# Optimization experiments

Hardware: AMD Instinct MI355X
Metric: run time of the kernel (lower is better)

The kernel has to match this reference:

```python
import jax, jax.numpy as jnp
import numpy as np

N = 16384
D = 512
VOCAB = 100000
EMB_SCALE = 0.05  # keep dot products ~O(1) so exp() is stable, like trained embeddings


def setup_inputs() -> dict:
    key = jax.random.key(0)
    k1, k2, k3, k4 = jax.random.split(key, 4)
    input_emb = jax.random.normal(k1, (N, D), dtype=jnp.float32) * EMB_SCALE
    target_emb = jax.random.normal(k2, (N, D), dtype=jnp.float32) * EMB_SCALE
    target_ids = jax.random.randint(k3, (N,), 0, VOCAB, dtype=jnp.int64) if jax.config.jax_enable_x64 else jax.random.randint(k3, (N,), 0, VOCAB, dtype=jnp.int32)
    # sampling probabilities in (eps, ~0.5) so 1 - q stays well away from 0
    q_probas = jax.random.uniform(k4, (N,), dtype=jnp.float32, minval=1e-4, maxval=0.5)
    # first half positives, second half negatives (static pattern, matches boolean-mask semantics)
    mask = jnp.arange(N) < (N // 2)
    return {"input_emb": input_emb, "target_emb": target_emb, "target_ids": target_ids,
            "q_probas": q_probas, "mask": mask}


def reference(input_emb, target_emb, target_ids, q_probas, mask):
    # mask is a constant selection pattern -> resolve to static index lists (jit-friendly shapes)
    mask_np = np.asarray(mask)
    pos_idx = np.nonzero(mask_np)[0]
    neg_idx = np.nonzero(~mask_np)[0]

    pos_emb = input_emb[pos_idx]                      # [P, D]
    pos_tgt = target_emb[pos_idx]                     # [P, D]
    neg_tgt = target_emb[neg_idx]                     # [Q, D]

    pos_sim = jnp.einsum('pd,pd->p', pos_emb, pos_tgt)          # [P]
    neg_sim = jnp.einsum('pd,qd->pq', pos_emb, neg_tgt)         # [P, Q]

    # accidental-hit mask: 1 where negative id differs from the positive's true id
    miss = (target_ids[pos_idx][:, None] != target_ids[neg_idx]).astype(jnp.float32)  # [P, Q]
    n_miss = jnp.sum(miss, axis=1, keepdims=True)                # [P, 1]

    # logQ correction: subtract log(n_miss * q_neg / (1 - q_pos))
    log_q = jnp.log(n_miss * q_probas[neg_idx][None, :] / (1.0 - q_probas[pos_idx][:, None]))
    neg_exp = jnp.exp(neg_sim - log_q)                           # [P, Q]
    neg_exp_sum = jnp.einsum('pq,pq->p', miss, neg_exp)          # [P]

    pos_exp = jnp.exp(pos_sim)
    batch_loss = jnp.mean(-pos_sim + jnp.log(pos_exp + neg_exp_sum))
    return batch_loss
```

## Files before the change

kernel.cpp:

```cpp
#include <hip/hip_runtime.h>
#include <hip/hip_bf16.h>

#define NPOS 8192
#define NNEG 8192
#define DIM  512
#define VOCAB 100000

#define FP8_SCALE 64.0f
#define ACC_DESCALE (1.0f / 4096.0f)

typedef float f32x4 __attribute__((ext_vector_type(4)));
typedef long  lng2  __attribute__((ext_vector_type(2)));

__device__ __forceinline__ void async_load16(const void* g, void* l) {
    __builtin_amdgcn_global_load_lds(
        (const __attribute__((address_space(1))) void*)g,
        (__attribute__((address_space(3))) void*)l, 16, 0, 0);
}

__global__ void prep_kernel(const float* __restrict__ input_emb,
                            const float* __restrict__ target_emb,
                            const int* __restrict__ ids,
                            const float* __restrict__ q_probas,
                            unsigned char* __restrict__ A8,
                            unsigned char* __restrict__ B8,
                            float* __restrict__ w, float* __restrict__ pos_sim,
                            int* __restrict__ hist) {
    const int r    = (blockIdx.x * blockDim.x + threadIdx.x) >> 6;
    const int lane = threadIdx.x & 63;

    const float4* ain = (const float4*)(input_emb  + (size_t)r * DIM);
    const float4* tin = (const float4*)(target_emb + (size_t)r * DIM);
    const float4* bin = (const float4*)(target_emb + (size_t)(NPOS + r) * DIM);

    float4 a0 = ain[lane * 2], a1 = ain[lane * 2 + 1];
    float4 t0 = tin[lane * 2], t1 = tin[lane * 2 + 1];
    float4 b0 = bin[lane * 2], b1 = bin[lane * 2 + 1];

    int alo = __builtin_amdgcn_cvt_pk_fp8_f32(a0.x * FP8_SCALE, a0.y * FP8_SCALE, 0, false);
    alo     = __builtin_amdgcn_cvt_pk_fp8_f32(a0.z * FP8_SCALE, a0.w * FP8_SCALE, alo, true);
    int ahi = __builtin_amdgcn_cvt_pk_fp8_f32(a1.x * FP8_SCALE, a1.y * FP8_SCALE, 0, false);
    ahi     = __builtin_amdgcn_cvt_pk_fp8_f32(a1.z * FP8_SCALE, a1.w * FP8_SCALE, ahi, true);
    int blo = __builtin_amdgcn_cvt_pk_fp8_f32(b0.x * FP8_SCALE, b0.y * FP8_SCALE, 0, false);
    blo     = __builtin_amdgcn_cvt_pk_fp8_f32(b0.z * FP8_SCALE, b0.w * FP8_SCALE, blo, true);
    int bhi = __builtin_amdgcn_cvt_pk_fp8_f32(b1.x * FP8_SCALE, b1.y * FP8_SCALE, 0, false);
    bhi     = __builtin_amdgcn_cvt_pk_fp8_f32(b1.z * FP8_SCALE, b1.w * FP8_SCALE, bhi, true);

    const int s = lane & 7, wnd = lane >> 3;
    const int phys = wnd * 64 + (s & 3) * 16 + (s >> 2) * 8;
    *(int2*)(A8 + (size_t)r * DIM + phys) = make_int2(alo, ahi);
    *(int2*)(B8 + (size_t)r * DIM + phys) = make_int2(blo, bhi);

    float sum = a0.x * t0.x + a0.y * t0.y + a0.z * t0.z + a0.w * t0.w
              + a1.x * t1.x + a1.y * t1.y + a1.z * t1.z + a1.w * t1.w;
    #pragma unroll
    for (int m = 32; m >= 1; m >>= 1) sum += __shfl_xor(sum, m);

    if (lane == 0) {
        pos_sim[r] = sum;
        w[r] = 1.0f / q_probas[NPOS + r];
        atomicAdd(&hist[ids[NPOS + r]], 1);
    }
}

__global__ __launch_bounds__(256) void gemm_kernel(
        const unsigned char* __restrict__ A8, const unsigned char* __restrict__ B8,
        const int* __restrict__ ids, const float* __restrict__ w,
        float* __restrict__ S) {
    __shared__ __align__(16) unsigned char Atile[2][128 * 64];
    __shared__ __align__(16) unsigned char Btile[2][128 * 64];

    const int tid  = threadIdx.x;
    const int lane = tid & 63;
    const int wv   = tid >> 6;
    const int wave_m = (wv & 1) * 64;
    const int wave_n = (wv >> 1) * 64;
    const int quad = lane >> 4;
    const int r16  = lane & 15;
    const int bm = blockIdx.x, bn = blockIdx.y;

    f32x4 acc[4][4] = {};

    const int srow_in = lane >> 2;
    const int sgran   = (lane & 3) ^ ((lane >> 3) & 3);
    const int row0 = wv * 32 + srow_in;
    const int row1 = wv * 32 + 16 + srow_in;
    const size_t goff0 = (size_t)row0 * DIM + sgran * 16;
    const size_t goff1 = (size_t)row1 * DIM + sgran * 16;
    const unsigned char* a_src = A8 + (size_t)(bm * 128) * DIM;
    const unsigned char* b_src = B8 + (size_t)(bn * 128) * DIM;
    const int ldst0 = (wv * 2) * 1024;
    const int ldst1 = (wv * 2 + 1) * 1024;

    async_load16(a_src + goff0, Atile[0] + ldst0);
    async_load16(a_src + goff1, Atile[0] + ldst1);
    async_load16(b_src + goff0, Btile[0] + ldst0);
    async_load16(b_src + goff1, Btile[0] + ldst1);
    __syncthreads();

    const int slot = quad ^ ((r16 >> 1) & 3);
    for (int it = 0; it < 8; ++it) {
        const int cur = it & 1;
        if (it < 7) {
            const size_t kb = (size_t)(it + 1) * 64;
            async_load16(a_src + kb + goff0, Atile[cur ^ 1] + ldst0);
            async_load16(a_src + kb + goff1, Atile[cur ^ 1] + ldst1);
            async_load16(b_src + kb + goff0, Btile[cur ^ 1] + ldst0);
            async_load16(b_src + kb + goff1, Btile[cur ^ 1] + ldst1);
        }

        lng2 af[4], bg[4];
        #pragma unroll
        for (int i = 0; i < 4; ++i) {
            const int arow = wave_m + i * 16 + r16;
            af[i] = *(const lng2*)(Atile[cur] + arow * 64 + slot * 16);
            const int brow = wave_n + i * 16 + r16;
            bg[i] = *(const lng2*)(Btile[cur] + brow * 64 + slot * 16);
        }
        #pragma unroll
        for (int i = 0; i < 4; ++i)
            #pragma unroll
            for (int j = 0; j < 4; ++j)
                acc[i][j] = __builtin_amdgcn_mfma_f32_16x16x32_fp8_fp8(af[i].x, bg[j].x, acc[i][j], 0, 0, 0);
        #pragma unroll
        for (int i = 0; i < 4; ++i)
            #pragma unroll
            for (int j = 0; j < 4; ++j)
                acc[i][j] = __builtin_amdgcn_mfma_f32_16x16x32_fp8_fp8(af[i].y, bg[j].y, acc[i][j], 0, 0, 0);

        if (it < 7) __syncthreads();
    }

    int idq[4]; float wq[4];
    #pragma unroll
    for (int j = 0; j < 4; ++j) {
        const int q = bn * 128 + wave_n + j * 16 + r16;
        idq[j] = ids[NPOS + q];
        wq[j]  = w[q];
    }
    #pragma unroll
    for (int i = 0; i < 4; ++i) {
        const int p0 = bm * 128 + wave_m + i * 16 + quad * 4;
        #pragma unroll
        for (int rr = 0; rr < 4; ++rr) {
            const int p = p0 + rr;
            const int idp = ids[p];
            float partial = 0.f;
            #pragma unroll
            for (int j = 0; j < 4; ++j) {
                const float e = __expf(acc[i][j][rr] * ACC_DESCALE) * wq[j];
                partial += (idp != idq[j]) ? e : 0.f;
            }
            partial += __shfl_xor(partial, 1);
            partial += __shfl_xor(partial, 2);
            partial += __shfl_xor(partial, 4);
            partial += __shfl_xor(partial, 8);
            if (r16 == 0) atomicAdd(&S[p], partial);
        }
    }
}

__global__ void final_kernel(const float* __restrict__ pos_sim,
                             const float* __restrict__ S,
                             const int* __restrict__ hist,
                             const int* __restrict__ ids,
                             const float* __restrict__ q_probas,
                             float* __restrict__ out) {
    __shared__ float red[256];
    float local = 0.f;
    for (int p = threadIdx.x; p < NPOS; p += 256) {
        const float ps  = pos_sim[p];
        const float n_miss = (float)(NNEG - hist[ids[p]]);
        const float nes = S[p] * (1.0f - q_probas[p]) / n_miss;
        local += -ps + logf(expf(ps) + nes);
    }
    red[threadIdx.x] = local;
    __syncthreads();
    #pragma unroll
    for (int s = 128; s > 0; s >>= 1) {
        if (threadIdx.x < s) red[threadIdx.x] += red[threadIdx.x + s];
        __syncthreads();
    }
    if (threadIdx.x == 0) out[0] = red[0] / (float)NPOS;
}

extern "C" void kernel_launch(void* const* d_in, const int* in_sizes, int n_in,
                              void* d_out, int out_size, void* d_ws, size_t ws_size,
                              hipStream_t stream) {
    const float* input_emb  = (const float*)d_in[0];
    const float* target_emb = (const float*)d_in[1];
    const int*   target_ids = (const int*)d_in[2];
    const float* q_probas   = (const float*)d_in[3];

    char* ws = (char*)d_ws;
    unsigned char* A8 = (unsigned char*)ws;
    unsigned char* B8 = (unsigned char*)(ws + (size_t)NPOS * DIM);
    float*  S       = (float*)(ws + (size_t)NPOS * DIM * 2);
    int*    hist    = (int*)(S + NPOS);
    float*  w       = (float*)(hist + VOCAB);
    float*  pos_sim = w + NPOS;

    hipMemsetAsync(S, 0, (size_t)(NPOS + VOCAB) * 4, stream);
    prep_kernel<<<2048, 256, 0, stream>>>(input_emb, target_emb, target_ids,
                                          q_probas, A8, B8, w, pos_sim, hist);
    gemm_kernel<<<dim3(64, 64), 256, 0, stream>>>(A8, B8, target_ids, w, S);
    final_kernel<<<1, 256, 0, stream>>>(pos_sim, S, hist, target_ids, q_probas, (float*)d_out);
}
```

Before: 208.7 us.

## Switch GEMM to scaled 32x32x64 FP8 MFMA with triple-buffered LDS pipeline

Replaces the 16x16x32 FP8 MFMA tiles with the MI355X block-scaled 32x32x64 f8f6f4 MFMA, using E8M0 scale operands to fold the descale into the instruction. The A/B FP8 layout written by the prep kernel becomes linear, and LDS reads use a new swizzle. The K loop moves from double to triple buffering with explicit vmcnt waits and a single barrier per step, plus setprio around the MFMAs. This aims to raise matrix throughput and cut synchronisation stalls, at the cost of more LDS use and correctness depending on the MFMA lane layout and the scale encoding.

```diff
diff --git a/kernel.cpp b/kernel.cpp
--- a/kernel.cpp
+++ b/kernel.cpp
@@ -7,10 +7,11 @@
 #define VOCAB 100000
 
 #define FP8_SCALE 64.0f
-#define ACC_DESCALE (1.0f / 4096.0f)
-
-typedef float f32x4 __attribute__((ext_vector_type(4)));
-typedef long  lng2  __attribute__((ext_vector_type(2)));
+#define SCALE_E8M0 0x79797979
+
+typedef int   i32x4  __attribute__((ext_vector_type(4)));
+typedef int   i32x8  __attribute__((ext_vector_type(8)));
+typedef float f32x16 __attribute__((ext_vector_type(16)));
 
 __device__ __forceinline__ void async_load16(const void* g, void* l) {
     __builtin_amdgcn_global_load_lds(
@@ -46,10 +47,8 @@
     int bhi = __builtin_amdgcn_cvt_pk_fp8_f32(b1.x * FP8_SCALE, b1.y * FP8_SCALE, 0, false);
     bhi     = __builtin_amdgcn_cvt_pk_fp8_f32(b1.z * FP8_SCALE, b1.w * FP8_SCALE, bhi, true);
 
-    const int s = lane & 7, wnd = lane >> 3;
-    const int phys = wnd * 64 + (s & 3) * 16 + (s >> 2) * 8;
-    *(int2*)(A8 + (size_t)r * DIM + phys) = make_int2(alo, ahi);
-    *(int2*)(B8 + (size_t)r * DIM + phys) = make_int2(blo, bhi);
+    *(int2*)(A8 + (size_t)r * DIM + lane * 8) = make_int2(alo, ahi);
+    *(int2*)(B8 + (size_t)r * DIM + lane * 8) = make_int2(blo, bhi);
 
     float sum = a0.x * t0.x + a0.y * t0.y + a0.z * t0.z + a0.w * t0.w
               + a1.x * t1.x + a1.y * t1.y + a1.z * t1.z + a1.w * t1.w;
@@ -67,19 +66,19 @@
         const unsigned char* __restrict__ A8, const unsigned char* __restrict__ B8,
         const int* __restrict__ ids, const float* __restrict__ w,
         float* __restrict__ S) {
-    __shared__ __align__(16) unsigned char Atile[2][128 * 64];
-    __shared__ __align__(16) unsigned char Btile[2][128 * 64];
+    __shared__ __align__(16) unsigned char Atile[3][128 * 64];
+    __shared__ __align__(16) unsigned char Btile[3][128 * 64];
 
     const int tid  = threadIdx.x;
     const int lane = tid & 63;
     const int wv   = tid >> 6;
     const int wave_m = (wv & 1) * 64;
     const int wave_n = (wv >> 1) * 64;
-    const int quad = lane >> 4;
-    const int r16  = lane & 15;
+    const int h    = lane >> 5;
+    const int r32  = lane & 31;
     const int bm = blockIdx.x, bn = blockIdx.y;
 
-    f32x4 acc[4][4] = {};
+    f32x16 acc[2][2] = {};
 
     const int srow_in = lane >> 2;
     const int sgran   = (lane & 3) ^ ((lane >> 3) & 3);
@@ -96,66 +95,86 @@
     async_load16(a_src + goff1, Atile[0] + ldst1);
     async_load16(b_src + goff0, Btile[0] + ldst0);
     async_load16(b_src + goff1, Btile[0] + ldst1);
-    __syncthreads();
-
-    const int slot = quad ^ ((r16 >> 1) & 3);
+    async_load16(a_src + 64 + goff0, Atile[1] + ldst0);
+    async_load16(a_src + 64 + goff1, Atile[1] + ldst1);
+    async_load16(b_src + 64 + goff0, Btile[1] + ldst0);
+    async_load16(b_src + 64 + goff1, Btile[1] + ldst1);
+
+    #pragma unroll
     for (int it = 0; it < 8; ++it) {
-        const int cur = it & 1;
-        if (it < 7) {
-            const size_t kb = (size_t)(it + 1) * 64;
-            async_load16(a_src + kb + goff0, Atile[cur ^ 1] + ldst0);
-            async_load16(a_src + kb + goff1, Atile[cur ^ 1] + ldst1);
-            async_load16(b_src + kb + goff0, Btile[cur ^ 1] + ldst0);
-            async_load16(b_src + kb + goff1, Btile[cur ^ 1] + ldst1);
+        if (it < 7) asm volatile("s_waitcnt vmcnt(4)" ::: "memory");
+        else        asm volatile("s_waitcnt vmcnt(0)" ::: "memory");
+        __builtin_amdgcn_s_barrier();
+
+        if (it < 6) {
+            const size_t kb = (size_t)(it + 2) * 64;
+            unsigned char* At = Atile[(it + 2) % 3];
+            unsigned char* Bt = Btile[(it + 2) % 3];
+            async_load16(a_src + kb + goff0, At + ldst0);
+            async_load16(a_src + kb + goff1, At + ldst1);
+            async_load16(b_src + kb + goff0, Bt + ldst0);
+            async_load16(b_src + kb + goff1, Bt + ldst1);
         }
 
-        lng2 af[4], bg[4];
+        const unsigned char* At = Atile[it % 3];
+        const unsigned char* Bt = Btile[it % 3];
+        i32x8 af[2], bg[2];
         #pragma unroll
-        for (int i = 0; i < 4; ++i) {
-            const int arow = wave_m + i * 16 + r16;
-            af[i] = *(const lng2*)(Atile[cur] + arow * 64 + slot * 16);
-            const int brow = wave_n + i * 16 + r16;
-            bg[i] = *(const lng2*)(Btile[cur] + brow * 64 + slot * 16);
+        for (int i = 0; i < 2; ++i) {
+            const int arow = wave_m + i * 32 + r32;
+            const int s0 = (((h << 1) ^ ((arow >> 1) & 3)) * 16);
+            const unsigned char* ap = At + arow * 64;
+            i32x4 alo = *(const i32x4*)(ap + s0);
+            i32x4 ahi = *(const i32x4*)(ap + (s0 ^ 16));
+            af[i].lo = alo; af[i].hi = ahi;
+            const int brow = wave_n + i * 32 + r32;
+            const int t0 = (((h << 1) ^ ((brow >> 1) & 3)) * 16);
+            const unsigned char* bp = Bt + brow * 64;
+            i32x4 blo = *(const i32x4*)(bp + t0);
+            i32x4 bhi = *(const i32x4*)(bp + (t0 ^ 16));
+            bg[i].lo = blo; bg[i].hi = bhi;
         }
+
+        __builtin_amdgcn_s_setprio(1);
         #pragma unroll
-        for (int i = 0; i < 4; ++i)
+        for (int i = 0; i < 2; ++i)
             #pragma unroll
-            for (int j = 0; j < 4; ++j)
-                acc[i][j] = __builtin_amdgcn_mfma_f32_16x16x32_fp8_fp8(af[i].x, bg[j].x, acc[i][j], 0, 0, 0);
-        #pragma unroll
-        for (int i = 0; i < 4; ++i)
-            #pragma unroll
-            for (int j = 0; j < 4; ++j)
-                acc[i][j] = __builtin_amdgcn_mfma_f32_16x16x32_fp8_fp8(af[i].y, bg[j].y, acc[i][j], 0, 0, 0);
-
-        if (it < 7) __syncthreads();
-    }
-
-    int idq[4]; float wq[4];
-    #pragma unroll
-    for (int j = 0; j < 4; ++j) {
-        const int q = bn * 128 + wave_n + j * 16 + r16;
+            for (int j = 0; j < 2; ++j)
+                acc[i][j] = __builtin_amdgcn_mfma_scale_f32_32x32x64_f8f6f4(
+                    af[i], bg[j], acc[i][j], 0, 0,
+                    0, SCALE_E8M0, 0, SCALE_E8M0);
+        __builtin_amdgcn_s_setprio(0);
+
+        asm volatile("s_waitcnt lgkmcnt(0)" ::: "memory");
+        __builtin_amdgcn_sched_barrier(0);
+    }
+
+    int idq[2]; float wq[2];
+    #pragma unroll
+    for (int j = 0; j < 2; ++j) {
+        const int q = bn * 128 + wave_n + j * 32 + r32;
         idq[j] = ids[NPOS + q];
         wq[j]  = w[q];
     }
     #pragma unroll
-    for (int i = 0; i < 4; ++i) {
-        const int p0 = bm * 128 + wave_m + i * 16 + quad * 4;
+    for (int i = 0; i < 2; ++i) {
+        const int p_base = bm * 128 + wave_m + i * 32 + 4 * h;
         #pragma unroll
-        for (int rr = 0; rr < 4; ++rr) {
-            const int p = p0 + rr;
+        for (int reg = 0; reg < 16; ++reg) {
+            const int p = p_base + (reg & 3) + 8 * (reg >> 2);
             const int idp = ids[p];
             float partial = 0.f;
             #pragma unroll
-            for (int j = 0; j < 4; ++j) {
-                const float e = __expf(acc[i][j][rr] * ACC_DESCALE) * wq[j];
+            for (int j = 0; j < 2; ++j) {
+                const float e = __expf(acc[i][j][reg]) * wq[j];
                 partial += (idp != idq[j]) ? e : 0.f;
             }
             partial += __shfl_xor(partial, 1);
             partial += __shfl_xor(partial, 2);
             partial += __shfl_xor(partial, 4);
             partial += __shfl_xor(partial, 8);
-            if (r16 == 0) atomicAdd(&S[p], partial);
+            partial += __shfl_xor(partial, 16);
+            if (r32 == 0) atomicAdd(&S[p], partial);
         }
     }
 }
```

After: 436.5 us. +109.1%, slower.

## Enlarge GEMM tile to 256x256 with 8 waves and ping-pong staged MFMA pipeline

Applied to the files above, without the earlier changes.

Doubles the block tile to 256x256 with 512 threads (8 waves, each owning 128x64), which halves global re-reads per output. The K loop is split into four MFMA phases separated by barriers, and async LDS loads for later k-tiles are interleaved between them, with s_setprio raising priority during MFMA bursts. The goal is to overlap loads with matrix math in a ping-pong style. It raises register pressure (acc[8][4]), doubles LDS use, and cuts the grid to 1024 blocks, which risks lower occupancy and more barrier overhead.

```diff
diff --git a/kernel.cpp b/kernel.cpp
--- a/kernel.cpp
+++ b/kernel.cpp
@@ -63,93 +63,128 @@
     }
 }
 
-__global__ __launch_bounds__(256) void gemm_kernel(
+__global__ __launch_bounds__(512, 2) void gemm_kernel(
         const unsigned char* __restrict__ A8, const unsigned char* __restrict__ B8,
         const int* __restrict__ ids, const float* __restrict__ w,
         float* __restrict__ S) {
-    __shared__ __align__(16) unsigned char Atile[2][128 * 64];
-    __shared__ __align__(16) unsigned char Btile[2][128 * 64];
+    __shared__ __align__(16) unsigned char Atile[2][256 * 64];
+    __shared__ __align__(16) unsigned char Btile[2][256 * 64];
 
     const int tid  = threadIdx.x;
     const int lane = tid & 63;
     const int wv   = tid >> 6;
-    const int wave_m = (wv & 1) * 64;
-    const int wave_n = (wv >> 1) * 64;
+    const int wm   = wv >> 2;
+    const int wn   = wv & 3;
     const int quad = lane >> 4;
     const int r16  = lane & 15;
     const int bm = blockIdx.x, bn = blockIdx.y;
 
-    f32x4 acc[4][4] = {};
-
-    const int srow_in = lane >> 2;
-    const int sgran   = (lane & 3) ^ ((lane >> 3) & 3);
-    const int row0 = wv * 32 + srow_in;
-    const int row1 = wv * 32 + 16 + srow_in;
-    const size_t goff0 = (size_t)row0 * DIM + sgran * 16;
-    const size_t goff1 = (size_t)row1 * DIM + sgran * 16;
-    const unsigned char* a_src = A8 + (size_t)(bm * 128) * DIM;
-    const unsigned char* b_src = B8 + (size_t)(bn * 128) * DIM;
-    const int ldst0 = (wv * 2) * 1024;
-    const int ldst1 = (wv * 2 + 1) * 1024;
-
-    async_load16(a_src + goff0, Atile[0] + ldst0);
-    async_load16(a_src + goff1, Atile[0] + ldst1);
-    async_load16(b_src + goff0, Btile[0] + ldst0);
-    async_load16(b_src + goff1, Btile[0] + ldst1);
-    __syncthreads();
+    f32x4 acc[8][4] = {};
+
+    const int srow  = (wv << 4) + (lane >> 2);
+    const int sgran = (lane & 3) ^ ((lane >> 3) & 3);
+    const unsigned char* a_base = A8 + (size_t)(bm * 256) * DIM;
+    const unsigned char* b_base = B8 + (size_t)(bn * 256) * DIM;
+
+#define STAGE_A(kt, h) async_load16(a_base + (size_t)((h)*128 + srow)*DIM + (kt)*64 + sgran*16, \
+                                    Atile[(kt)&1] + (h)*8192 + (wv<<10))
+#define STAGE_B(kt, h) async_load16(b_base + (size_t)((h)*128 + srow)*DIM + (kt)*64 + sgran*16, \
+                                    Btile[(kt)&1] + (h)*8192 + (wv<<10))
+
+    STAGE_A(0, 0); STAGE_A(0, 1); STAGE_B(0, 0); STAGE_B(0, 1);
+    STAGE_A(1, 0); STAGE_B(1, 0); STAGE_B(1, 1);
+    asm volatile("s_waitcnt vmcnt(3)" ::: "memory");
+    __builtin_amdgcn_s_barrier();
 
     const int slot = quad ^ ((r16 >> 1) & 3);
-    for (int it = 0; it < 8; ++it) {
-        const int cur = it & 1;
-        if (it < 7) {
-            const size_t kb = (size_t)(it + 1) * 64;
-            async_load16(a_src + kb + goff0, Atile[cur ^ 1] + ldst0);
-            async_load16(a_src + kb + goff1, Atile[cur ^ 1] + ldst1);
-            async_load16(b_src + kb + goff0, Btile[cur ^ 1] + ldst0);
-            async_load16(b_src + kb + goff1, Btile[cur ^ 1] + ldst1);
-        }
-
-        lng2 af[4], bg[4];
-        #pragma unroll
-        for (int i = 0; i < 4; ++i) {
-            const int arow = wave_m + i * 16 + r16;
-            af[i] = *(const lng2*)(Atile[cur] + arow * 64 + slot * 16);
-            const int brow = wave_n + i * 16 + r16;
-            bg[i] = *(const lng2*)(Btile[cur] + brow * 64 + slot * 16);
-        }
-        #pragma unroll
-        for (int i = 0; i < 4; ++i)
-            #pragma unroll
-            for (int j = 0; j < 4; ++j)
-                acc[i][j] = __builtin_amdgcn_mfma_f32_16x16x32_fp8_fp8(af[i].x, bg[j].x, acc[i][j], 0, 0, 0);
-        #pragma unroll
-        for (int i = 0; i < 4; ++i)
-            #pragma unroll
-            for (int j = 0; j < 4; ++j)
-                acc[i][j] = __builtin_amdgcn_mfma_f32_16x16x32_fp8_fp8(af[i].y, bg[j].y, acc[i][j], 0, 0, 0);
-
-        if (it < 7) __syncthreads();
-    }
+    lng2 af03[4], af47[4], bg[4];
+
+    #pragma unroll
+    for (int kt = 0; kt < 8; ++kt) {
+        const unsigned char* At = Atile[kt & 1];
+        const unsigned char* Bt = Btile[kt & 1];
+
+        #pragma unroll
+        for (int f = 0; f < 4; ++f)
+            af03[f] = *(const lng2*)(At + (wm*128 + f*16 + r16)*64 + slot*16);
+        #pragma unroll
+        for (int n = 0; n < 4; ++n)
+            bg[n] = *(const lng2*)(Bt + (wn*64 + n*16 + r16)*64 + slot*16);
+        if (kt < 7) STAGE_A(kt + 1, 1);
+        __builtin_amdgcn_s_barrier();
+        asm volatile("s_waitcnt lgkmcnt(0)" ::: "memory");
+        __builtin_amdgcn_sched_barrier(0);
+        __builtin_amdgcn_s_setprio(1);
+        #pragma unroll
+        for (int f = 0; f < 4; ++f)
+            #pragma unroll
+            for (int n = 0; n < 4; ++n)
+                acc[f][n] = __builtin_amdgcn_mfma_f32_16x16x32_fp8_fp8(af03[f].x, bg[n].x, acc[f][n], 0, 0, 0);
+        __builtin_amdgcn_s_setprio(0);
+        __builtin_amdgcn_s_barrier();
+
+        #pragma unroll
+        for (int f = 0; f < 4; ++f)
+            af47[f] = *(const lng2*)(At + (wm*128 + (f+4)*16 + r16)*64 + slot*16);
+        if (kt < 6) STAGE_B(kt + 2, 0);
+        __builtin_amdgcn_s_barrier();
+        asm volatile("s_waitcnt lgkmcnt(0)" ::: "memory");
+        __builtin_amdgcn_sched_barrier(0);
+        __builtin_amdgcn_s_setprio(1);
+        #pragma unroll
+        for (int f = 0; f < 4; ++f)
+            #pragma unroll
+            for (int n = 0; n < 4; ++n)
+                acc[f+4][n] = __builtin_amdgcn_mfma_f32_16x16x32_fp8_fp8(af47[f].x, bg[n].x, acc[f+4][n], 0, 0, 0);
+        __builtin_amdgcn_s_setprio(0);
+        __builtin_amdgcn_s_barrier();
+
+        if (kt < 6) STAGE_B(kt + 2, 1);
+        __builtin_amdgcn_s_barrier();
+        __builtin_amdgcn_s_setprio(1);
+        #pragma unroll
+        for (int f = 0; f < 4; ++f)
+            #pragma unroll
+            for (int n = 0; n < 4; ++n)
+                acc[f][n] = __builtin_amdgcn_mfma_f32_16x16x32_fp8_fp8(af03[f].y, bg[n].y, acc[f][n], 0, 0, 0);
+        __builtin_amdgcn_s_setprio(0);
+        __builtin_amdgcn_s_barrier();
+
+        if (kt < 6) STAGE_A(kt + 2, 0);
+        __builtin_amdgcn_s_barrier();
+        __builtin_amdgcn_s_setprio(1);
+        #pragma unroll
+        for (int f = 0; f < 4; ++f)
+            #pragma unroll
+            for (int n = 0; n < 4; ++n)
+                acc[f+4][n] = __builtin_amdgcn_mfma_f32_16x16x32_fp8_fp8(af47[f].y, bg[n].y, acc[f+4][n], 0, 0, 0);
+        __builtin_amdgcn_s_setprio(0);
+        if (kt < 6)       asm volatile("s_waitcnt vmcnt(3)" ::: "memory");
+        else if (kt == 6) asm volatile("s_waitcnt vmcnt(0)" ::: "memory");
+        __builtin_amdgcn_s_barrier();
+    }
+#undef STAGE_A
+#undef STAGE_B
 
     int idq[4]; float wq[4];
     #pragma unroll
-    for (int j = 0; j < 4; ++j) {
-        const int q = bn * 128 + wave_n + j * 16 + r16;
-        idq[j] = ids[NPOS + q];
-        wq[j]  = w[q];
-    }
-    #pragma unroll
-    for (int i = 0; i < 4; ++i) {
-        const int p0 = bm * 128 + wave_m + i * 16 + quad * 4;
+    for (int n = 0; n < 4; ++n) {
+        const int q = bn * 256 + wn * 64 + n * 16 + r16;
+        idq[n] = ids[NPOS + q];
+        wq[n]  = w[q];
+    }
+    #pragma unroll
+    for (int f = 0; f < 8; ++f) {
+        const int p0r = bm * 256 + wm * 128 + f * 16 + quad * 4;
         #pragma unroll
         for (int rr = 0; rr < 4; ++rr) {
-            const int p = p0 + rr;
+            const int p = p0r + rr;
             const int idp = ids[p];
             float partial = 0.f;
             #pragma unroll
-            for (int j = 0; j < 4; ++j) {
-                const float e = __expf(acc[i][j][rr] * ACC_DESCALE) * wq[j];
-                partial += (idp != idq[j]) ? e : 0.f;
+            for (int n = 0; n < 4; ++n) {
+                const float e = __expf(acc[f][n][rr] * ACC_DESCALE) * wq[n];
+                partial += (idp != idq[n]) ? e : 0.f;
             }
             partial += __shfl_xor(partial, 1);
             partial += __shfl_xor(partial, 2);
@@ -203,6 +238,6 @@
     hipMemsetAsync(S, 0, (size_t)(NPOS + VOCAB) * 4, stream);
     prep_kernel<<<2048, 256, 0, stream>>>(input_emb, target_emb, target_ids,
                                           q_probas, A8, B8, w, pos_sim, hist);
-    gemm_kernel<<<dim3(64, 64), 256, 0, stream>>>(A8, B8, target_ids, w, S);
+    gemm_kernel<<<dim3(32, 32), 512, 0, stream>>>(A8, B8, target_ids, w, S);
     final_kernel<<<1, 256, 0, stream>>>(pos_sim, S, hist, target_ids, q_probas, (float*)d_out);
 }
```

New measurement: 235.7 us. 1.13x slower.
